# Kernel tuning notes

Hardware: AMD Instinct MI355X
Metric: run time of the kernel (lower is better)

The kernel has to match this reference:

```python
import jax, jax.numpy as jnp
import numpy as np

K = 2
ALPHA = 1.0
EPS = 1e-6


def _bce_logits(x, z):
    # binary_cross_entropy_with_logits, elementwise, numerically stable
    return jax.nn.softplus(x) - x * z


def _unfold(x, i):
    # F.unfold(x, kernel_size=2i+1, padding=i) for x: [B,1,H,W] -> [B, P, H*W]
    ks = 2 * i + 1
    p = jax.lax.conv_general_dilated_patches(
        x, (ks, ks), (1, 1), [(i, i), (i, i)])  # [B, ks*ks, H, W], zero-padded
    B = x.shape[0]
    return p.reshape(B, ks * ks, -1)


def setup_inputs() -> dict:
    key = jax.random.key(0)
    k1, k2 = jax.random.split(key)
    B, H, W = 8, 512, 512
    pred = jax.random.normal(k1, (B, 1, H, W), dtype=jnp.float32)
    target = jax.random.randint(k2, (B, 1, H, W), 0, 2).astype(jnp.float32)
    return {"pred": pred, "target": target}


def reference(pred, target):
    B, _, H, W = pred.shape
    N = H * W
    bce = _bce_logits(pred, target).reshape(B, 1, N)  # [B,1,N]
    total = jnp.zeros((B, N), dtype=pred.dtype)
    for i in range(1, K + 1):
        ks = 2 * i + 1
        P = ks * ks
        c = P // 2
        up = _unfold(pred, i)                      # [B,P,N]
        ut = _unfold(target, i)                    # [B,P,N]
        vm = _unfold(jnp.ones_like(target), i) == 0  # True where padding
        cp = up[:, c:c + 1, :]                     # center logits [B,1,N]
        ct = ut[:, c:c + 1, :]
        joint = cp * up
        lab = ct * ut
        mutual = _bce_logits(joint, lab)
        pairwise = jnp.exp(-jax.nn.sigmoid(cp) * jax.nn.sigmoid(up))
        loss = bce / (mutual + ALPHA * pairwise + EPS)
        loss = jnp.where(vm, jnp.asarray(1.0, loss.dtype), loss)
        total = total + (0.5 ** (i - 1)) * (loss.sum(axis=1) / P)
    return total.mean()
```

## Files before the change

kernel.cpp:

```cpp
#include <hip/hip_runtime.h>

#define TILE 32
#define HALO 2
#define LH (TILE + HALO)
#define LW (TILE + 2 * HALO)
#define EPS 1e-6f


__device__ __forceinline__ float softplus_f(float x) {
    return fmaxf(x, 0.f) + __logf(1.f + __expf(-fabsf(x)));
}

constexpr float W_IN  = 1.0f / 9.0f + 0.02f;
constexpr float W_OUT = 0.02f;

__constant__ const int   c_dy[12] = {0, 0, 1, 1, 1, 1, 1, 2, 2, 2, 2, 2};
__constant__ const int   c_dx[12] = {1, 2, -2, -1, 0, 1, 2, -2, -1, 0, 1, 2};
__constant__ const float c_w[12]  = {W_IN, W_OUT, W_OUT, W_IN, W_IN, W_IN,
                                     W_OUT, W_OUT, W_OUT, W_OUT, W_OUT, W_OUT};

__global__ __launch_bounds__(256) void scloss_main(
    const float* __restrict__ pred, const float* __restrict__ target,
    double* __restrict__ partial, int B, int H, int W) {
    __shared__ float4 sh[LH * LW];

    const int tilesX = W / TILE;
    const int tilesPer = tilesX * (H / TILE);
    const int b = blockIdx.x / tilesPer;
    const int tile = blockIdx.x % tilesPer;
    const int ty0 = (tile / tilesX) * TILE;
    const int tx0 = (tile % tilesX) * TILE;

    const float* pbase = pred + (size_t)b * H * W;
    const float* tbase = target + (size_t)b * H * W;
    const int tid = threadIdx.x;

    for (int idx = tid; idx < LH * LW; idx += 256) {
        const int cy = idx / LW, cx = idx % LW;
        const int gy = ty0 + cy;
        const int gx = tx0 + cx - HALO;
        float p = 0.f, t = 0.f, g = -1.f, bce = 0.f;
        if (gy < H && gx >= 0 && gx < W) {
            p = pbase[gy * W + gx];
            t = tbase[gy * W + gx];
            g = __fdividef(1.f, 1.f + __expf(-p));
            bce = softplus_f(p) - p * t;
        }
        sh[idx] = make_float4(p, t, g, bce);
    }
    __syncthreads();

    const int px = tid & 31;
    const int py0 = tid >> 5;
    float acc = 0.f;

    const bool negCheck = (ty0 == 0) || (tx0 == 0) || (tx0 + TILE == W);

    constexpr int pdy[12] = {0, 0, 1, 1, 1, 1, 1, 2, 2, 2, 2, 2};
    constexpr int pdx[12] = {1, 2, -2, -1, 0, 1, 2, -2, -1, 0, 1, 2};
    constexpr float pw12[12] = {W_IN, W_OUT, W_OUT, W_IN, W_IN, W_IN,
                                W_OUT, W_OUT, W_OUT, W_OUT, W_OUT, W_OUT};

    #pragma unroll
    for (int r = 0; r < 4; ++r) {
        const int ay = py0 + r * 8;
        const float4* base = &sh[ay * LW + px + HALO];
        const float4 ca = base[0];

        {
            const float j = ca.x * ca.x;
            const float m = softplus_f(j) - j * (ca.y * ca.y);
            const float pw = __expf(-ca.z * ca.z);
            acc += __fdividef(W_IN * ca.w, m + pw + EPS);
        }

        #pragma unroll
        for (int k = 0; k < 12; ++k) {
            const float w = pw12[k];
            const float4 cb = base[pdy[k] * LW + pdx[k]];
            const float j = ca.x * cb.x;
            const float m = softplus_f(j) - j * (ca.y * cb.y);
            const float pw = __expf(-ca.z * cb.z);
            const float pv = __fdividef(w * (ca.w + cb.w), m + pw + EPS);
            acc += (cb.z < 0.f) ? w : pv;
        }

        if (negCheck) {
            const int gy = ty0 + ay, gx = tx0 + px;
            #pragma unroll
            for (int k = 0; k < 12; ++k) {
                const int ny = gy - c_dy[k], nx = gx - c_dx[k];
                if (ny < 0 || nx < 0 || nx >= W) acc += c_w[k];
            }
        }
    }

    #pragma unroll
    for (int off = 32; off > 0; off >>= 1)
        acc += __shfl_down(acc, off, 64);
    __shared__ double wsum[4];
    if ((tid & 63) == 0) wsum[tid >> 6] = (double)acc;
    __syncthreads();
    if (tid == 0)
        partial[blockIdx.x] = wsum[0] + wsum[1] + wsum[2] + wsum[3];
}

__global__ __launch_bounds__(256) void scloss_reduce(
    const double* __restrict__ partial, int n, float* __restrict__ out,
    double inv_cnt) {
    __shared__ double sm[256];
    double s = 0.0;
    for (int i = threadIdx.x; i < n; i += 256) s += partial[i];
    sm[threadIdx.x] = s;
    __syncthreads();
    for (int off = 128; off > 0; off >>= 1) {
        if (threadIdx.x < off) sm[threadIdx.x] += sm[threadIdx.x + off];
        __syncthreads();
    }
    if (threadIdx.x == 0) out[0] = (float)(sm[0] * inv_cnt);
}

extern "C" void kernel_launch(void* const* d_in, const int* in_sizes, int n_in,
                              void* d_out, int out_size, void* d_ws, size_t ws_size,
                              hipStream_t stream) {
    const float* pred   = (const float*)d_in[0];
    const float* target = (const float*)d_in[1];
    float* out = (float*)d_out;

    const int H = 512, W = 512;
    const int B = in_sizes[0] / (H * W);

    double* partial = (double*)d_ws;
    const int nblocks = B * (H / TILE) * (W / TILE);

    scloss_main<<<nblocks, 256, 0, stream>>>(pred, target, partial, B, H, W);
    scloss_reduce<<<1, 256, 0, stream>>>(partial, nblocks, out,
                                         1.0 / ((double)B * H * W));
}
```

Before: 104.1 us.

## Replace transcendentals with polynomials, merge divisions, and fuse the final reduction

The softplus log term and the pairwise exponential are replaced with low-order polynomial approximations over their bounded input ranges. The thirteen per-pixel fractions are combined into a single numerator/denominator tree, so only one reciprocal is needed instead of thirteen divides. Padding is now handled by an explicit edge-correction path instead of a per-neighbor sentinel select. The separate reduce kernel is replaced by a memset plus per-block float atomicAdd, with sizes hardcoded. These changes cut SFU and divide work and one launch, at the cost of approximation error, possible overflow or underflow in the merged fraction products, and non-deterministic float accumulation.

```diff
diff --git a/kernel.cpp b/kernel.cpp
--- a/kernel.cpp
+++ b/kernel.cpp
@@ -4,49 +4,80 @@
 #define HALO 2
 #define LH (TILE + HALO)
 #define LW (TILE + 2 * HALO)
-#define EPS 1e-6f
-
-
-__device__ __forceinline__ float softplus_f(float x) {
-    return fmaxf(x, 0.f) + __logf(1.f + __expf(-fabsf(x)));
-}
+#define HT 512
+#define WD 512
 
 constexpr float W_IN  = 1.0f / 9.0f + 0.02f;
 constexpr float W_OUT = 0.02f;
+constexpr float LN15C = 0.40546611f;
+constexpr float INV_D_OOB = 0.59037527f;
 
-__constant__ const int   c_dy[12] = {0, 0, 1, 1, 1, 1, 1, 2, 2, 2, 2, 2};
-__constant__ const int   c_dx[12] = {1, 2, -2, -1, 0, 1, 2, -2, -1, 0, 1, 2};
-__constant__ const float c_w[12]  = {W_IN, W_OUT, W_OUT, W_IN, W_IN, W_IN,
-                                     W_OUT, W_OUT, W_OUT, W_OUT, W_OUT, W_OUT};
+struct Frac { float n, d; };
+__device__ __forceinline__ Frac fmerge(Frac a, Frac b) {
+    Frac r;
+    r.n = __builtin_fmaf(a.n, b.d, b.n * a.d);
+    r.d = a.d * b.d;
+    return r;
+}
+
+__device__ __forceinline__ Frac pairf(const float4 ca, const float4 cb, float w) {
+    const float j = ca.x * cb.x;
+    const float u = __expf(-fabsf(j));
+    const float t = __builtin_fmaf(u, 0.66666667f, -0.33333333f);
+    float L = __builtin_fmaf(0.33333333f, t, -0.5f);
+    L = __builtin_fmaf(L, t, 1.0f);
+    L = __builtin_fmaf(L, t, LN15C);
+    const float m = __builtin_fmaf(-j, ca.y * cb.y, fmaxf(j, 0.f)) + L;
+    const float z = __builtin_fmaf(ca.z, cb.z, -0.5f);
+    float E = __builtin_fmaf(-0.16666667f, z, 0.5f);
+    E = __builtin_fmaf(E, z, -1.0f);
+    E = __builtin_fmaf(E, z, 1.0f);
+    Frac r;
+    r.d = __builtin_fmaf(E, 0.60653066f, m);
+    r.n = (ca.w + cb.w) * w;
+    return r;
+}
 
 __global__ __launch_bounds__(256) void scloss_main(
     const float* __restrict__ pred, const float* __restrict__ target,
-    double* __restrict__ partial, int B, int H, int W) {
+    float* __restrict__ out, double inv_cnt) {
     __shared__ float4 sh[LH * LW];
 
-    const int tilesX = W / TILE;
-    const int tilesPer = tilesX * (H / TILE);
-    const int b = blockIdx.x / tilesPer;
-    const int tile = blockIdx.x % tilesPer;
-    const int ty0 = (tile / tilesX) * TILE;
-    const int tx0 = (tile % tilesX) * TILE;
+    const int b = blockIdx.x >> 8;
+    const int tile = blockIdx.x & 255;
+    const int ty0 = (tile >> 4) << 5;
+    const int tx0 = (tile & 15) << 5;
 
-    const float* pbase = pred + (size_t)b * H * W;
-    const float* tbase = target + (size_t)b * H * W;
+    const float* pbase = pred + ((size_t)b << 18);
+    const float* tbase = target + ((size_t)b << 18);
     const int tid = threadIdx.x;
 
-    for (int idx = tid; idx < LH * LW; idx += 256) {
-        const int cy = idx / LW, cx = idx % LW;
-        const int gy = ty0 + cy;
-        const int gx = tx0 + cx - HALO;
-        float p = 0.f, t = 0.f, g = -1.f, bce = 0.f;
-        if (gy < H && gx >= 0 && gx < W) {
-            p = pbase[gy * W + gx];
-            t = tbase[gy * W + gx];
-            g = __fdividef(1.f, 1.f + __expf(-p));
-            bce = softplus_f(p) - p * t;
+    int cy = tid / LW;
+    int cx = tid - cy * LW;
+    #pragma unroll
+    for (int i = 0; i < 5; ++i) {
+        const int idx = tid + (i << 8);
+        if (idx < LH * LW) {
+            const int gy = ty0 + cy;
+            const int gx = tx0 + cx - HALO;
+            float p = 0.f, t = 0.f, g = 0.f, bce = 0.f;
+            if ((unsigned)gx < (unsigned)WD && gy < HT) {
+                const int gi = (gy << 9) + gx;
+                p = pbase[gi];
+                t = tbase[gi];
+                const float en = __expf(-fabsf(p));
+                const float inv = __builtin_amdgcn_rcpf(1.f + en);
+                g = (p >= 0.f) ? inv : en * inv;
+                const float tt = __builtin_fmaf(en, 0.66666667f, -0.33333333f);
+                float L = __builtin_fmaf(0.33333333f, tt, -0.5f);
+                L = __builtin_fmaf(L, tt, 1.0f);
+                L = __builtin_fmaf(L, tt, 0.40546511f);
+                bce = __builtin_fmaf(-p, t, fmaxf(p, 0.f)) + L;
+            }
+            sh[idx] = make_float4(p, t, g, bce);
         }
-        sh[idx] = make_float4(p, t, g, bce);
+        cx += 4; cy += 7;
+        if (cx >= LW) { cx -= LW; ++cy; }
     }
     __syncthreads();
 
@@ -54,7 +85,7 @@
     const int py0 = tid >> 5;
     float acc = 0.f;
 
-    const bool negCheck = (ty0 == 0) || (tx0 == 0) || (tx0 + TILE == W);
+    const bool edge = (tx0 == 0) | (tx0 == WD - TILE) | (ty0 == 0) | (ty0 == HT - TILE);
 
     constexpr int pdy[12] = {0, 0, 1, 1, 1, 1, 1, 2, 2, 2, 2, 2};
     constexpr int pdx[12] = {1, 2, -2, -1, 0, 1, 2, -2, -1, 0, 1, 2};
@@ -63,34 +94,39 @@
 
     #pragma unroll
     for (int r = 0; r < 4; ++r) {
-        const int ay = py0 + r * 8;
+        const int ay = py0 + (r << 3);
         const float4* base = &sh[ay * LW + px + HALO];
         const float4 ca = base[0];
 
-        {
-            const float j = ca.x * ca.x;
-            const float m = softplus_f(j) - j * (ca.y * ca.y);
-            const float pw = __expf(-ca.z * ca.z);
-            acc += __fdividef(W_IN * ca.w, m + pw + EPS);
-        }
+        const Frac f0 = pairf(ca, ca, W_IN * 0.5f);
+        const Frac f1 = pairf(ca, base[1],          W_IN);
+        const Frac f2 = pairf(ca, base[2],          W_OUT);
+        const Frac f3 = pairf(ca, base[LW - 2],     W_OUT);
+        const Frac f4 = pairf(ca, base[LW - 1],     W_IN);
+        const Frac f5 = pairf(ca, base[LW],         W_IN);
+        const Frac f6 = pairf(ca, base[LW + 1],     W_IN);
+        const Frac f7 = pairf(ca, base[LW + 2],     W_OUT);
+        const Frac f8 = pairf(ca, base[2 * LW - 2], W_OUT);
+        const Frac f9 = pairf(ca, base[2 * LW - 1], W_OUT);
+        const Frac fA = pairf(ca, base[2 * LW],     W_OUT);
+        const Frac fB = pairf(ca, base[2 * LW + 1], W_OUT);
+        const Frac fC = pairf(ca, base[2 * LW + 2], W_OUT);
 
-        #pragma unroll
-        for (int k = 0; k < 12; ++k) {
-            const float w = pw12[k];
-            const float4 cb = base[pdy[k] * LW + pdx[k]];
-            const float j = ca.x * cb.x;
-            const float m = softplus_f(j) - j * (ca.y * cb.y);
-            const float pw = __expf(-ca.z * cb.z);
-            const float pv = __fdividef(w * (ca.w + cb.w), m + pw + EPS);
-            acc += (cb.z < 0.f) ? w : pv;
-        }
+        const Frac a0 = fmerge(f0, f1), a1 = fmerge(f2, f3), a2 = fmerge(f4, f5);
+        const Frac a3 = fmerge(f6, f7), a4 = fmerge(f8, f9), a5 = fmerge(fA, fB);
+        const Frac b0 = fmerge(a0, a1), b1 = fmerge(a2, a3), b2 = fmerge(a4, a5);
+        const Frac c0 = fmerge(b0, b1), c1 = fmerge(b2, fC);
+        const Frac d0 = fmerge(c0, c1);
+        acc = __builtin_fmaf(d0.n, __builtin_amdgcn_rcpf(d0.d), acc);
 
-        if (negCheck) {
+        if (edge) {
             const int gy = ty0 + ay, gx = tx0 + px;
             #pragma unroll
             for (int k = 0; k < 12; ++k) {
-                const int ny = gy - c_dy[k], nx = gx - c_dx[k];
-                if (ny < 0 || nx < 0 || nx >= W) acc += c_w[k];
+                if (gy + pdy[k] >= HT || gx + pdx[k] < 0 || gx + pdx[k] >= WD)
+                    acc += pw12[k] * (1.f - ca.w * INV_D_OOB);
+                if (gy - pdy[k] < 0 || gx - pdx[k] < 0 || gx - pdx[k] >= WD)
+                    acc += pw12[k];
             }
         }
     }
@@ -101,23 +137,10 @@
     __shared__ double wsum[4];
     if ((tid & 63) == 0) wsum[tid >> 6] = (double)acc;
     __syncthreads();
-    if (tid == 0)
-        partial[blockIdx.x] = wsum[0] + wsum[1] + wsum[2] + wsum[3];
-}
-
-__global__ __launch_bounds__(256) void scloss_reduce(
-    const double* __restrict__ partial, int n, float* __restrict__ out,
-    double inv_cnt) {
-    __shared__ double sm[256];
-    double s = 0.0;
-    for (int i = threadIdx.x; i < n; i += 256) s += partial[i];
-    sm[threadIdx.x] = s;
-    __syncthreads();
-    for (int off = 128; off > 0; off >>= 1) {
-        if (threadIdx.x < off) sm[threadIdx.x] += sm[threadIdx.x + off];
-        __syncthreads();
+    if (tid == 0) {
+        const double s = wsum[0] + wsum[1] + wsum[2] + wsum[3];
+        atomicAdd(out, (float)(s * inv_cnt));
     }
-    if (threadIdx.x == 0) out[0] = (float)(sm[0] * inv_cnt);
 }
 
 extern "C" void kernel_launch(void* const* d_in, const int* in_sizes, int n_in,
@@ -127,13 +150,10 @@
     const float* target = (const float*)d_in[1];
     float* out = (float*)d_out;
 
-    const int H = 512, W = 512;
-    const int B = in_sizes[0] / (H * W);
+    const int B = in_sizes[0] / (HT * WD);
+    const int nblocks = B * 256;
 
-    double* partial = (double*)d_ws;
-    const int nblocks = B * (H / TILE) * (W / TILE);
-
-    scloss_main<<<nblocks, 256, 0, stream>>>(pred, target, partial, B, H, W);
-    scloss_reduce<<<1, 256, 0, stream>>>(partial, nblocks, out,
-                                         1.0 / ((double)B * H * W));
+    hipMemsetAsync(out, 0, sizeof(float), stream);
+    scloss_main<<<nblocks, 256, 0, stream>>>(pred, target, out,
+                                             1.0 / ((double)B * HT * WD));
 }
```

Result: faster. 100.1 us (-3.8%).
